# Kernel tuning notes

Measured on AMD Instinct MI355X. Metric: run time of the kernel, lower is better.

The kernel has to match this reference:

```python
import jax, jax.numpy as jnp
import numpy as np

B, S, D, H = 4, 2048, 768, 12
DK = D // H


def setup_inputs() -> dict:
    key = jax.random.key(0)
    ks = jax.random.split(key, 5)
    sc = 0.02
    return {
        "x": jax.random.normal(ks[0], (B, S, D), dtype=jnp.float32),
        "wq": jax.random.normal(ks[1], (D, D), dtype=jnp.float32) * sc,
        "bq": jnp.zeros((D,), dtype=jnp.float32),
        "wk": jax.random.normal(ks[2], (D, D), dtype=jnp.float32) * sc,
        "bk": jnp.zeros((D,), dtype=jnp.float32),
        "wv": jax.random.normal(ks[3], (D, D), dtype=jnp.float32) * sc,
        "bv": jnp.zeros((D,), dtype=jnp.float32),
        "wo": jax.random.normal(ks[4], (D, D), dtype=jnp.float32) * sc,
        "bo": jnp.zeros((D,), dtype=jnp.float32),
    }


def reference(x, wq, bq, wk, bk, wv, bv, wo, bo):
    b, s, d = x.shape
    # torch nn.Linear: y = x @ W.T + b
    q = (x @ wq.T + bq).reshape(b, s, H, DK).transpose(0, 2, 1, 3)  # [b,h,s,dk]
    k = (x @ wk.T + bk).reshape(b, s, H, DK).transpose(0, 2, 1, 3)
    v = (x @ wv.T + bv).reshape(b, s, H, DK).transpose(0, 2, 1, 3)
    scale = 1.0 / np.sqrt(DK).astype(np.float32)
    scores = jnp.einsum("bhqd,bhkd->bhqk", q, k) * scale  # [b,h,s,s]
    causal = jnp.triu(jnp.ones((s, s), dtype=bool), k=1)  # True above diagonal -> masked
    scores = jnp.where(causal[None, None], jnp.float32(-jnp.inf), scores)
    probs = jax.nn.softmax(scores, axis=-1)
    attn = jnp.einsum("bhqk,bhkd->bhqd", probs, v)  # [b,h,s,dk]
    attn = attn.transpose(0, 2, 1, 3).reshape(b, s, d)
    return attn @ wo.T + bo
```

## Files before the change

kernel.cpp:

```cpp
#include <hip/hip_runtime.h>
#include <hip/hip_bf16.h>
#include <cstdint>

static constexpr int B_ = 4, S_ = 2048, D_ = 768, H_ = 12, DK_ = 64;
static constexpr int M_ = B_ * S_;

typedef short bf16x4 __attribute__((ext_vector_type(4)));
typedef short bf16x8 __attribute__((ext_vector_type(8)));
typedef float f32x4 __attribute__((ext_vector_type(4)));
typedef float f32x16 __attribute__((ext_vector_type(16)));
typedef int i32x4 __attribute__((ext_vector_type(4)));

#define MFMA16(a, b, c) __builtin_amdgcn_mfma_f32_16x16x32_bf16((a), (b), (c), 0, 0, 0)
#define MFMA32(a, b, c) __builtin_amdgcn_mfma_f32_32x32x16_bf16((a), (b), (c), 0, 0, 0)

__device__ inline ushort f2bf(float f) {
  uint32_t u = __float_as_uint(f);
  u += 0x7fffu + ((u >> 16) & 1u);
  return (ushort)(u >> 16);
}
__device__ inline uint32_t pkbf(float a, float b) {
  return (uint32_t)f2bf(a) | ((uint32_t)f2bf(b) << 16);
}
__device__ inline uint32_t cvtpk(float lo, float hi) {
  uint32_t r;
  asm("v_cvt_pk_bf16_f32 %0, %1, %2" : "=v"(r) : "v"(lo), "v"(hi));
  return r;
}
__device__ inline float fexp2(float x) {
  float r;
  asm("v_exp_f32 %0, %1" : "=v"(r) : "v"(x));
  return r;
}
__device__ inline void gload_lds16(const void* g, void* l) {
  __builtin_amdgcn_global_load_lds((const __attribute__((address_space(1))) void*)g,
                                   (__attribute__((address_space(3))) void*)l, 16, 0, 0);
}

__global__ void cvt_f32_bf16(const float* __restrict__ in, ushort* __restrict__ out, int n8) {
  int i = blockIdx.x * 256 + threadIdx.x;
  if (i >= n8) return;
  const float4* p = (const float4*)in;
  float4 v0 = p[2 * i], v1 = p[2 * i + 1];
  ((uint4*)out)[i] = make_uint4(pkbf(v0.x, v0.y), pkbf(v0.z, v0.w),
                                pkbf(v1.x, v1.y), pkbf(v1.z, v1.w));
}

__global__ void cvtw_f32_bf16(const float* __restrict__ w0, const float* __restrict__ w1,
                              const float* __restrict__ w2, const float* __restrict__ w3,
                              ushort* __restrict__ o0, ushort* __restrict__ o1,
                              ushort* __restrict__ o2, ushort* __restrict__ o3, int n8) {
  const float* in;
  ushort* out;
  switch (blockIdx.y) {
    case 0: in = w0; out = o0; break;
    case 1: in = w1; out = o1; break;
    case 2: in = w2; out = o2; break;
    default: in = w3; out = o3; break;
  }
  int i = blockIdx.x * 256 + threadIdx.x;
  if (i >= n8) return;
  const float4* p = (const float4*)in;
  float4 v0 = p[2 * i], v1 = p[2 * i + 1];
  ((uint4*)out)[i] = make_uint4(pkbf(v0.x, v0.y), pkbf(v0.z, v0.w),
                                pkbf(v1.x, v1.y), pkbf(v1.z, v1.w));
}

__global__ __launch_bounds__(256) void gemm_qkv(const ushort* __restrict__ A,
                                                const ushort* __restrict__ Wq,
                                                const ushort* __restrict__ Wk,
                                                const ushort* __restrict__ Wv,
                                                const float* __restrict__ bqp,
                                                const float* __restrict__ bkp,
                                                const float* __restrict__ bvp,
                                                ushort* __restrict__ Qo,
                                                ushort* __restrict__ Ko,
                                                ushort* __restrict__ Vo) {
  constexpr int K = D_;
  constexpr int BK = 64;
  constexpr int NT = K / BK;
  __shared__ ushort SMEM[24576];
  ushort* Asb = SMEM;
  ushort* Bsb = SMEM + 8192;

  const int wsel = blockIdx.y / 6;
  const int bn = (blockIdx.y % 6) * 128;
  const ushort* Bw = wsel == 0 ? Wq : wsel == 1 ? Wk : Wv;
  const float* bias = wsel == 0 ? bqp : wsel == 1 ? bkp : bvp;
  ushort* outp = wsel == 0 ? Qo : wsel == 1 ? Ko : Vo;
  const float qscale = wsel == 0 ? 0.125f * 1.4426950408889634f : 1.0f;

  const int tid = threadIdx.x;
  const int lane = tid & 63, w = tid >> 6;
  const int wr = w >> 1, wc = w & 1;
  const int l15 = lane & 15, l4 = lane >> 4;
  const int bm = blockIdx.x * 64;

  const char* Ac = (const char*)A;
  const char* Bc = (const char*)Bw;

  f32x4 acc[2][4] = {};

  auto stage = [&](int buf, int k0) {
#pragma unroll
    for (int i = 0; i < 2; ++i) {
      int o = (i * 256 + tid) * 16;
      int r = o >> 7, c = o & 127;
      int cs = c ^ ((r & 7) << 4);
      gload_lds16(Ac + ((size_t)(bm + r) * K + k0) * 2 + cs,
                  (char*)(Asb + buf * 4096) + o);
    }
#pragma unroll
    for (int i = 0; i < 4; ++i) {
      int o = (i * 256 + tid) * 16;
      int r = o >> 7, c = o & 127;
      int cs = c ^ ((r & 7) << 4);
      gload_lds16(Bc + ((size_t)(bn + r) * K + k0) * 2 + cs,
                  (char*)(Bsb + buf * 8192) + o);
    }
  };

  stage(0, 0);
  __syncthreads();
  int cur = 0;
  for (int t = 0; t < NT; ++t) {
    if (t + 1 < NT) stage(cur ^ 1, (t + 1) * BK);
    const char* Ab = (const char*)(Asb + cur * 4096);
    const char* Bb = (const char*)(Bsb + cur * 8192);
    bf16x8 a[2][2], b[2][4];
#pragma unroll
    for (int kc = 0; kc < 2; ++kc) {
#pragma unroll
      for (int mi = 0; mi < 2; ++mi) {
        int row = wr * 32 + mi * 16 + l15;
        int col = (kc * 64 + l4 * 16) ^ ((row & 7) << 4);
        a[kc][mi] = *(const bf16x8*)(Ab + row * 128 + col);
      }
#pragma unroll
      for (int ni = 0; ni < 4; ++ni) {
        int row = wc * 64 + ni * 16 + l15;
        int col = (kc * 64 + l4 * 16) ^ ((row & 7) << 4);
        b[kc][ni] = *(const bf16x8*)(Bb + row * 128 + col);
      }
    }
    __builtin_amdgcn_s_setprio(1);
    if (wsel < 2) {
#pragma unroll
      for (int kc = 0; kc < 2; ++kc)
#pragma unroll
        for (int mi = 0; mi < 2; ++mi)
#pragma unroll
          for (int ni = 0; ni < 4; ++ni)
            acc[mi][ni] = MFMA16(a[kc][mi], b[kc][ni], acc[mi][ni]);
    } else {
#pragma unroll
      for (int kc = 0; kc < 2; ++kc)
#pragma unroll
        for (int mi = 0; mi < 2; ++mi)
#pragma unroll
          for (int ni = 0; ni < 4; ++ni)
            acc[mi][ni] = MFMA16(b[kc][ni], a[kc][mi], acc[mi][ni]);
    }
    __builtin_amdgcn_s_setprio(0);
    __syncthreads();
    cur ^= 1;
  }

  ushort* Cst = SMEM;
#pragma unroll
  for (int ni = 0; ni < 4; ++ni) {
    float bv[4];
    if (wsel < 2) {
      float bc = bias[bn + wc * 64 + ni * 16 + l15];
#pragma unroll
      for (int r = 0; r < 4; ++r) bv[r] = bc;
    } else {
#pragma unroll
      for (int r = 0; r < 4; ++r) bv[r] = bias[bn + wc * 64 + ni * 16 + l4 * 4 + r];
    }
#pragma unroll
    for (int mi = 0; mi < 2; ++mi)
#pragma unroll
      for (int r = 0; r < 4; ++r) {
        float v = (acc[mi][ni][r] + bv[r]) * qscale;
        if (wsel < 2) {
          int lr = wr * 32 + mi * 16 + l4 * 4 + r;
          int lc = wc * 64 + ni * 16 + l15;
          Cst[lr * 128 + (lc ^ ((lr & 3) << 4))] = f2bf(v);
        } else {
          int lr = wc * 64 + ni * 16 + l4 * 4 + r;
          int lc = wr * 32 + mi * 16 + l15;
          Cst[lr * 64 + (lc ^ ((lr & 3) << 4))] = f2bf(v);
        }
      }
  }
  __syncthreads();
  const int bbV = bm >> 11;
#pragma unroll
  for (int it = 0; it < 4; ++it) {
    int chunk = it * 256 + tid;
    if (wsel < 2) {
      int lr = chunk >> 4, cc = chunk & 15;
      i32x4 v = *(const i32x4*)&Cst[lr * 128 + ((cc * 8) ^ ((lr & 3) << 4))];
      int gr = bm + lr;
      int b0 = gr >> 11, s = gr & 2047;
      int gc = bn + cc * 8;
      int h = gc >> 6, dk0 = gc & 63;
      *(i32x4*)&outp[((((size_t)b0 * H_ + h) * S_ + s) << 6) + dk0] = v;
    } else {
      int lr = chunk >> 3, cc = chunk & 7;
      i32x4 v = *(const i32x4*)&Cst[lr * 64 + ((cc * 8) ^ ((lr & 3) << 4))];
      int gn = bn + lr;
      int h = gn >> 6, dk = gn & 63;
      int s0 = (bm & 2047) + cc * 8;
      *(i32x4*)&outp[(((size_t)bbV * H_ + h) * 64 + dk) * S_ + s0] = v;
    }
  }
}

__global__ __launch_bounds__(256) void gemm_out(const ushort* __restrict__ A,
                                                const ushort* __restrict__ Bw,
                                                const float* __restrict__ bias,
                                                float* __restrict__ outp) {
  constexpr int K = D_;
  constexpr int BK = 64;
  constexpr int NT = K / BK;
  __shared__ ushort SMEM[24576];
  ushort* Asb = SMEM;
  ushort* Bsb = SMEM + 8192;

  const int tid = threadIdx.x;
  const int lane = tid & 63, w = tid >> 6;
  const int wr = w >> 1, wc = w & 1;
  const int l15 = lane & 15, l4 = lane >> 4;
  const int bm = blockIdx.x * 64, bn = blockIdx.y * 128;

  const char* Ac = (const char*)A;
  const char* Bc = (const char*)Bw;

  f32x4 acc[2][4] = {};

  auto stage = [&](int buf, int k0) {
#pragma unroll
    for (int i = 0; i < 2; ++i) {
      int o = (i * 256 + tid) * 16;
      int r = o >> 7, c = o & 127;
      int cs = c ^ ((r & 7) << 4);
      gload_lds16(Ac + ((size_t)(bm + r) * K + k0) * 2 + cs,
                  (char*)(Asb + buf * 4096) + o);
    }
#pragma unroll
    for (int i = 0; i < 4; ++i) {
      int o = (i * 256 + tid) * 16;
      int r = o >> 7, c = o & 127;
      int cs = c ^ ((r & 7) << 4);
      gload_lds16(Bc + ((size_t)(bn + r) * K + k0) * 2 + cs,
                  (char*)(Bsb + buf * 8192) + o);
    }
  };

  stage(0, 0);
  __syncthreads();
  int cur = 0;
  for (int t = 0; t < NT; ++t) {
    if (t + 1 < NT) stage(cur ^ 1, (t + 1) * BK);
    const char* Ab = (const char*)(Asb + cur * 4096);
    const char* Bb = (const char*)(Bsb + cur * 8192);
    bf16x8 a[2][2], b[2][4];
#pragma unroll
    for (int kc = 0; kc < 2; ++kc) {
#pragma unroll
      for (int mi = 0; mi < 2; ++mi) {
        int row = wr * 32 + mi * 16 + l15;
        int col = (kc * 64 + l4 * 16) ^ ((row & 7) << 4);
        a[kc][mi] = *(const bf16x8*)(Ab + row * 128 + col);
      }
#pragma unroll
      for (int ni = 0; ni < 4; ++ni) {
        int row = wc * 64 + ni * 16 + l15;
        int col = (kc * 64 + l4 * 16) ^ ((row & 7) << 4);
        b[kc][ni] = *(const bf16x8*)(Bb + row * 128 + col);
      }
    }
    __builtin_amdgcn_s_setprio(1);
#pragma unroll
    for (int kc = 0; kc < 2; ++kc)
#pragma unroll
      for (int mi = 0; mi < 2; ++mi)
#pragma unroll
        for (int ni = 0; ni < 4; ++ni)
          acc[mi][ni] = MFMA16(a[kc][mi], b[kc][ni], acc[mi][ni]);
    __builtin_amdgcn_s_setprio(0);
    __syncthreads();
    cur ^= 1;
  }

#pragma unroll
  for (int mi = 0; mi < 2; ++mi)
#pragma unroll
    for (int ni = 0; ni < 4; ++ni) {
      int col = bn + wc * 64 + ni * 16 + l15;
      float bv = bias[col];
#pragma unroll
      for (int r = 0; r < 4; ++r) {
        int row = bm + wr * 32 + mi * 16 + l4 * 4 + r;
        outp[(size_t)row * D_ + col] = acc[mi][ni][r] + bv;
      }
    }
}

__global__ __launch_bounds__(512) void attn_fwd5(const ushort* __restrict__ Q,
                                                 const ushort* __restrict__ Kg,
                                                 const ushort* __restrict__ Vt,
                                                 ushort* __restrict__ Oa) {
  __shared__ ushort KVb[2][2][64 * 64];
  __shared__ float Ll[4][32];

  const int bh = blockIdx.x;
  const int w = threadIdx.x >> 6, lane = threadIdx.x & 63;
  const int l31 = lane & 31, hi = lane >> 5;
  const int pair = w >> 1, sp = w & 1;
  const int qtb = gridDim.y - 1 - blockIdx.y;
  const int qb = qtb * 128;
  const int q0 = qb + pair * 32;

  const ushort* Qb = Q + (size_t)bh * (S_ * DK_);
  const char* Kc = (const char*)(Kg + (size_t)bh * (S_ * DK_));
  const char* Vc = (const char*)(Vt + (size_t)bh * (DK_ * S_));
  char* kKT = (char*)&KVb[0][0][0];
  char* kVT = (char*)&KVb[1][0][0];

  bf16x8 qf[4];
#pragma unroll
  for (int kc = 0; kc < 4; ++kc)
    qf[kc] = *(const bf16x8*)&Qb[(q0 + l31) * 64 + kc * 16 + hi * 8];

  f32x16 ot[2] = {};
  float l = 0.f;

  const int obase = w * 1024;
  const int o = obase + lane * 16;
  const int mk = ((o >> 7) & 7) << 4;
  const char* kap = Kc + (o ^ mk);
  const char* vap = Vc + (size_t)(o >> 7) * 4096 + ((o & 127) ^ mk);

  auto stage = [&](int buf, int kt) {
    const size_t k0 = (size_t)kt * 64;
    gload_lds16(kap + k0 * 128, kKT + buf * 8192 + obase);
    gload_lds16(vap + k0 * 2, kVT + buf * 8192 + obase);
  };

  const int nkt = qb / 64 + 2;
  int cur = 0;
  stage(0, 0);
  __syncthreads();

  for (int kt = 0; kt < nkt; ++kt) {
    if (kt + 1 < nkt) stage(cur ^ 1, kt + 1);
    const int ks = kt * 64 + sp * 32;
    if (ks <= q0 + 31) {
      const char* KTc = kKT + cur * 8192;
      const char* VTc = kVT + cur * 8192;
      f32x16 st = {};
      __builtin_amdgcn_s_setprio(1);
#pragma unroll
      for (int kc = 0; kc < 4; ++kc) {
        int row = sp * 32 + l31;
        int col = (kc * 32 + hi * 16) ^ ((row & 7) << 4);
        bf16x8 kf = *(const bf16x8*)(KTc + row * 128 + col);
        st = MFMA32(kf, qf[kc], st);
      }
      __builtin_amdgcn_s_setprio(0);
      if (ks + 31 > q0) {
#pragma unroll
        for (int r = 0; r < 16; ++r) {
          int kr = ks + (r & 3) + 8 * (r >> 2) + 4 * hi;
          if (kr > q0 + l31) st[r] = -__builtin_inff();
        }
      }
#pragma unroll
      for (int r = 0; r < 16; ++r) st[r] = fexp2(st[r]);
      float sx[8];
#pragma unroll
      for (int i = 0; i < 8; ++i) sx[i] = st[i] + st[i + 8];
#pragma unroll
      for (int i = 0; i < 4; ++i) sx[i] = sx[i] + sx[i + 4];
      float rs = (sx[0] + sx[1]) + (sx[2] + sx[3]);
      rs += __shfl_xor(rs, 32, 64);
      l += rs;
#pragma unroll
      for (int c = 0; c < 2; ++c) {
        i32x4 bw;
        bw.x = (int)cvtpk(st[8 * c + 0], st[8 * c + 1]);
        bw.y = (int)cvtpk(st[8 * c + 2], st[8 * c + 3]);
        bw.z = (int)cvtpk(st[8 * c + 4], st[8 * c + 5]);
        bw.w = (int)cvtpk(st[8 * c + 6], st[8 * c + 7]);
        bf16x8 pf = __builtin_bit_cast(bf16x8, bw);
        __builtin_amdgcn_s_setprio(1);
#pragma unroll
        for (int t = 0; t < 2; ++t) {
          int row = t * 32 + l31;
          int swz = (row & 7) << 4;
          int colA = sp * 64 + c * 32 + hi * 8;
          bf16x4 vlo = *(const bf16x4*)(VTc + row * 128 + (colA ^ swz));
          bf16x4 vhi = *(const bf16x4*)(VTc + row * 128 + ((colA + 16) ^ swz));
          bf16x8 vf = __builtin_shufflevector(vlo, vhi, 0, 1, 2, 3, 4, 5, 6, 7);
          ot[t] = MFMA32(vf, pf, ot[t]);
        }
        __builtin_amdgcn_s_setprio(0);
      }
    }
    __syncthreads();
    cur ^= 1;
  }

  float* Om = (float*)&KVb[0][0][0];
  if (sp == 0) {
#pragma unroll
    for (int t = 0; t < 2; ++t)
#pragma unroll
      for (int r = 0; r < 16; ++r) {
        int d = (r & 3) + 8 * (r >> 2) + 4 * hi + 32 * t;
        Om[(pair * 64 + d) * 32 + l31] = ot[t][r];
      }
    if (hi == 0) Ll[pair][l31] = l;
  }
  __syncthreads();
  if (sp == 1) {
    float inv = 1.0f / (l + Ll[pair][l31]);
#pragma unroll
    for (int t = 0; t < 2; ++t)
#pragma unroll
      for (int r = 0; r < 16; ++r) {
        int d = (r & 3) + 8 * (r >> 2) + 4 * hi + 32 * t;
        ot[t][r] = (ot[t][r] + Om[(pair * 64 + d) * 32 + l31]) * inv;
      }
    uint32_t* Ow = (uint32_t*)&Om[pair * 64 * 32];
#pragma unroll
    for (int t = 0; t < 2; ++t)
#pragma unroll
      for (int g = 0; g < 4; ++g)
#pragma unroll
        for (int rp = 0; rp < 2; ++rp) {
          int r0 = 4 * g + 2 * rp;
          int ucol = rp + 4 * g + 2 * hi + 16 * t;
          Ow[l31 * 32 + (ucol ^ ((l31 & 7) << 2))] = cvtpk(ot[t][r0], ot[t][r0 + 1]);
        }
    const int bb = bh / H_, h = bh % H_;
#pragma unroll
    for (int i = 0; i < 4; ++i) {
      int chunk = i * 64 + lane;
      int q = chunk >> 3, cc = chunk & 7;
      i32x4 v = *(const i32x4*)&Ow[q * 32 + ((cc * 4) ^ ((q & 7) << 2))];
      *(i32x4*)&Oa[((size_t)bb * S_ + q0 + q) * D_ + h * 64 + cc * 8] = v;
    }
  }
}

extern "C" void kernel_launch(void* const* d_in, const int* in_sizes, int n_in,
                              void* d_out, int out_size, void* d_ws, size_t ws_size,
                              hipStream_t stream) {
  const float* x  = (const float*)d_in[0];
  const float* wq = (const float*)d_in[1];
  const float* bq = (const float*)d_in[2];
  const float* wk = (const float*)d_in[3];
  const float* bk = (const float*)d_in[4];
  const float* wv = (const float*)d_in[5];
  const float* bv = (const float*)d_in[6];
  const float* wo = (const float*)d_in[7];
  const float* bo = (const float*)d_in[8];

  const size_t XB = (size_t)M_ * D_;
  const size_t WB = (size_t)D_ * D_;
  ushort* xb    = (ushort*)d_ws;
  ushort* wqb   = xb + XB;
  ushort* wkb   = wqb + WB;
  ushort* wvb   = wkb + WB;
  ushort* wob   = wvb + WB;
  ushort* qb    = wob + WB;
  ushort* kbuf  = qb + XB;
  ushort* vtb   = kbuf + XB;
  ushort* attnb = vtb + XB;

  cvt_f32_bf16<<<(int)(XB / 8 / 256), 256, 0, stream>>>(x, xb, (int)(XB / 8));
  cvtw_f32_bf16<<<dim3((int)(WB / 8 / 256), 4), 256, 0, stream>>>(
      wq, wk, wv, wo, wqb, wkb, wvb, wob, (int)(WB / 8));

  gemm_qkv<<<dim3(M_ / 64, 18), 256, 0, stream>>>(xb, wqb, wkb, wvb,
                                                  bq, bk, bv, qb, kbuf, vtb);
  attn_fwd5<<<dim3(B_ * H_, S_ / 128), 512, 0, stream>>>(qb, kbuf, vtb, attnb);
  gemm_out<<<dim3(M_ / 64, D_ / 128), 256, 0, stream>>>(attnb, wob, bo, (float*)d_out);
}
```

Measured before the change: 108.9 us.

## Fuse fp32-to-bf16 conversion of x into QKV GEMM A-tile loading

Removes the separate x conversion kernel and its bf16 workspace buffer. The QKV GEMM now loads fp32 x tiles into registers, converts them with v_cvt_pk_bf16_f32 and writes them swizzled into LDS, overlapping the next tile's global load with the current MFMA work. This saves a kernel launch and a write plus re-read of x in bf16. In exchange, each of the 18 column blocks reads twice the A bytes in fp32, uses more registers, and adds VALU and LDS-store work inside the loop.

New measurement: 132.7 us. +21.9%, slower.

```diff
diff --git a/kernel.cpp b/kernel.cpp
--- a/kernel.cpp
+++ b/kernel.cpp
@@ -10,6 +10,7 @@
 typedef float f32x4 __attribute__((ext_vector_type(4)));
 typedef float f32x16 __attribute__((ext_vector_type(16)));
 typedef int i32x4 __attribute__((ext_vector_type(4)));
+typedef uint32_t u32x2 __attribute__((ext_vector_type(2)));
 
 #define MFMA16(a, b, c) __builtin_amdgcn_mfma_f32_16x16x32_bf16((a), (b), (c), 0, 0, 0)
 #define MFMA32(a, b, c) __builtin_amdgcn_mfma_f32_32x32x16_bf16((a), (b), (c), 0, 0, 0)
@@ -35,15 +36,6 @@
 __device__ inline void gload_lds16(const void* g, void* l) {
   __builtin_amdgcn_global_load_lds((const __attribute__((address_space(1))) void*)g,
                                    (__attribute__((address_space(3))) void*)l, 16, 0, 0);
-}
-
-__global__ void cvt_f32_bf16(const float* __restrict__ in, ushort* __restrict__ out, int n8) {
-  int i = blockIdx.x * 256 + threadIdx.x;
-  if (i >= n8) return;
-  const float4* p = (const float4*)in;
-  float4 v0 = p[2 * i], v1 = p[2 * i + 1];
-  ((uint4*)out)[i] = make_uint4(pkbf(v0.x, v0.y), pkbf(v0.z, v0.w),
-                                pkbf(v1.x, v1.y), pkbf(v1.z, v1.w));
 }
 
 __global__ void cvtw_f32_bf16(const float* __restrict__ w0, const float* __restrict__ w1,
@@ -66,7 +58,7 @@
                                 pkbf(v1.x, v1.y), pkbf(v1.z, v1.w));
 }
 
-__global__ __launch_bounds__(256) void gemm_qkv(const ushort* __restrict__ A,
+__global__ __launch_bounds__(256) void gemm_qkv(const float* __restrict__ Xf,
                                                 const ushort* __restrict__ Wq,
                                                 const ushort* __restrict__ Wk,
                                                 const ushort* __restrict__ Wv,
@@ -96,20 +88,33 @@
   const int l15 = lane & 15, l4 = lane >> 4;
   const int bm = blockIdx.x * 64;
 
-  const char* Ac = (const char*)A;
   const char* Bc = (const char*)Bw;
 
   f32x4 acc[2][4] = {};
-
-  auto stage = [&](int buf, int k0) {
-#pragma unroll
-    for (int i = 0; i < 2; ++i) {
+  f32x4 areg[4];
+
+  auto loadA = [&](int k0) {
+#pragma unroll
+    for (int i = 0; i < 4; ++i) {
       int o = (i * 256 + tid) * 16;
-      int r = o >> 7, c = o & 127;
-      int cs = c ^ ((r & 7) << 4);
-      gload_lds16(Ac + ((size_t)(bm + r) * K + k0) * 2 + cs,
-                  (char*)(Asb + buf * 4096) + o);
-    }
+      int r = o >> 8, cB = o & 255;
+      areg[i] = *(const f32x4*)((const char*)Xf +
+                                ((size_t)(bm + r) * K) * 4 + (size_t)k0 * 4 + cB);
+    }
+  };
+  auto writeA = [&](int buf) {
+#pragma unroll
+    for (int i = 0; i < 4; ++i) {
+      int o = (i * 256 + tid) * 16;
+      int r = o >> 8, c2 = (o & 255) >> 1;
+      int d = (r * 128 + c2) ^ ((r & 7) << 4);
+      u32x2 pk;
+      pk.x = cvtpk(areg[i][0], areg[i][1]);
+      pk.y = cvtpk(areg[i][2], areg[i][3]);
+      *(u32x2*)((char*)(Asb + buf * 4096) + d) = pk;
+    }
+  };
+  auto stageB = [&](int buf, int k0) {
 #pragma unroll
     for (int i = 0; i < 4; ++i) {
       int o = (i * 256 + tid) * 16;
@@ -120,11 +125,16 @@
     }
   };
 
-  stage(0, 0);
+  loadA(0);
+  stageB(0, 0);
+  writeA(0);
   __syncthreads();
   int cur = 0;
   for (int t = 0; t < NT; ++t) {
-    if (t + 1 < NT) stage(cur ^ 1, (t + 1) * BK);
+    if (t + 1 < NT) {
+      stageB(cur ^ 1, (t + 1) * BK);
+      loadA((t + 1) * BK);
+    }
     const char* Ab = (const char*)(Asb + cur * 4096);
     const char* Bb = (const char*)(Bsb + cur * 8192);
     bf16x8 a[2][2], b[2][4];
@@ -162,6 +172,7 @@
             acc[mi][ni] = MFMA16(b[kc][ni], a[kc][mi], acc[mi][ni]);
     }
     __builtin_amdgcn_s_setprio(0);
+    if (t + 1 < NT) writeA(cur ^ 1);
     __syncthreads();
     cur ^= 1;
   }
@@ -472,8 +483,7 @@
 
   const size_t XB = (size_t)M_ * D_;
   const size_t WB = (size_t)D_ * D_;
-  ushort* xb    = (ushort*)d_ws;
-  ushort* wqb   = xb + XB;
+  ushort* wqb   = (ushort*)d_ws;
   ushort* wkb   = wqb + WB;
   ushort* wvb   = wkb + WB;
   ushort* wob   = wvb + WB;
@@ -482,11 +492,10 @@
   ushort* vtb   = kbuf + XB;
   ushort* attnb = vtb + XB;
 
-  cvt_f32_bf16<<<(int)(XB / 8 / 256), 256, 0, stream>>>(x, xb, (int)(XB / 8));
   cvtw_f32_bf16<<<dim3((int)(WB / 8 / 256), 4), 256, 0, stream>>>(
       wq, wk, wv, wo, wqb, wkb, wvb, wob, (int)(WB / 8));
 
-  gemm_qkv<<<dim3(M_ / 64, 18), 256, 0, stream>>>(xb, wqb, wkb, wvb,
+  gemm_qkv<<<dim3(M_ / 64, 18), 256, 0, stream>>>(x, wqb, wkb, wvb,
                                                   bq, bk, bv, qb, kbuf, vtb);
   attn_fwd5<<<dim3(B_ * H_, S_ / 128), 512, 0, stream>>>(qb, kbuf, vtb, attnb);
   gemm_out<<<dim3(M_ / 64, D_ / 128), 256, 0, stream>>>(attnb, wob, bo, (float*)d_out);
```
